# Kernel optimization log

Measured on AMD Instinct MI355X. Metric: run time of the kernel, lower is better.

The kernel has to match this reference:

```python
import jax, jax.numpy as jnp
import numpy as np

N_NODES = 100000
N_EDGES = 1600000
D_IN = 128
D_OUT = 128


def setup_inputs() -> dict:
    key = jax.random.key(0)
    k1, k2, k3, k4, k5 = jax.random.split(key, 5)
    h = jax.random.normal(k1, (N_NODES, D_IN), dtype=jnp.float32)
    src = jax.random.randint(k2, (N_EDGES,), 0, N_NODES, dtype=jnp.int64)
    dst = jax.random.randint(k3, (N_EDGES,), 0, N_NODES, dtype=jnp.int64)
    # Glorot-ish init for linear weights (PyTorch nn.Linear style: [out, in])
    scale = 1.0 / np.sqrt(D_IN)
    W_self = jax.random.uniform(k4, (D_OUT, D_IN), jnp.float32, -scale, scale)
    W_neigh = jax.random.uniform(k5, (D_OUT, D_IN), jnp.float32, -scale, scale)
    b = jnp.zeros((D_OUT,), dtype=jnp.float32)
    return {"h": h, "src": src, "dst": dst, "W_self": W_self,
            "W_neigh": W_neigh, "b": b}


def reference(h, src, dst, W_self, W_neigh, b):
    n_nodes = h.shape[0]
    # neighbor gather + segment-mean over in-neighbors (DGL fn.copy_u + fn.mean)
    msg = h[src]                                            # [E, D_in]
    neigh_sum = jax.ops.segment_sum(msg, dst, num_segments=n_nodes)
    deg = jax.ops.segment_sum(jnp.ones_like(dst, dtype=h.dtype), dst,
                              num_segments=n_nodes)         # [N]
    h_neigh = neigh_sum / jnp.maximum(deg, 1.0)[:, None]    # mean; 0 for isolated
    # SAGEConv mean: fc_self(h) + fc_neigh(h_neigh) + bias
    out = h @ W_self.T + h_neigh @ W_neigh.T + b
    return out
```

## Files before the change

kernel.cpp:

```cpp
#include <hip/hip_runtime.h>
#include <stdint.h>

#define NN 100000
#define NE 1600000
#define DD 128
#define NTILES ((NN + 127) / 128)
#define NB 256
#define CHUNK (NE / NB)
#define NBUCK ((NN + 255) / 256)
#define GH_N (NBUCK * NB)
#define GH_BLK (GH_N / 256)

typedef __bf16 bf16x8 __attribute__((ext_vector_type(8)));
typedef float f32x4 __attribute__((ext_vector_type(4)));
typedef float f32x2 __attribute__((ext_vector_type(2)));

__device__ __forceinline__ unsigned int f2bf2(float a, float b) {
  union { float f; unsigned u; } x, y;
  x.f = a; y.f = b;
  unsigned ua = x.u + (0x7FFFu + ((x.u >> 16) & 1u));
  unsigned ub = y.u + (0x7FFFu + ((y.u >> 16) & 1u));
  return (ua >> 16) | (ub & 0xFFFF0000u);
}

__global__ __launch_bounds__(256) void convert_hist_kernel(
    const float4* __restrict__ hp, uint2* __restrict__ h8,
    const int* __restrict__ dst, int* __restrict__ gh) {
  __shared__ int lh[NBUCK];
  int gid = blockIdx.x * 256 + threadIdx.x;
  float4 a = hp[2 * gid], b = hp[2 * gid + 1];
  int lo = __builtin_amdgcn_cvt_pk_fp8_f32(a.x, a.y, 0, false);
  lo = __builtin_amdgcn_cvt_pk_fp8_f32(a.z, a.w, lo, true);
  int hi = __builtin_amdgcn_cvt_pk_fp8_f32(b.x, b.y, 0, false);
  hi = __builtin_amdgcn_cvt_pk_fp8_f32(b.z, b.w, hi, true);
  h8[gid] = make_uint2((unsigned)lo, (unsigned)hi);

  if (blockIdx.x < NB) {
    int t = threadIdx.x, bb = blockIdx.x;
    for (int i = t; i < NBUCK; i += 256) lh[i] = 0;
    __syncthreads();
    int e0 = bb * CHUNK;
    for (int e = e0 + t; e < e0 + CHUNK; e += 256)
      atomicAdd(&lh[dst[e] >> 8], 1);
    __syncthreads();
    for (int i = t; i < NBUCK; i += 256) gh[i * NB + bb] = lh[i];
  }
}

__global__ __launch_bounds__(256) void blocksum_kernel(const int* __restrict__ gh,
                                                       int* __restrict__ bsum) {
  __shared__ int s[256];
  int t = threadIdx.x;
  s[t] = gh[blockIdx.x * 256 + t];
  __syncthreads();
  for (int d = 128; d > 0; d >>= 1) {
    if (t < d) s[t] += s[t + d];
    __syncthreads();
  }
  if (t == 0) bsum[blockIdx.x] = s[0];
}

__global__ __launch_bounds__(512) void scanbsum_kernel(const int* __restrict__ bsum,
                                                       int* __restrict__ bsum_ex) {
  __shared__ int s[512];
  int t = threadIdx.x;
  int v = (t < GH_BLK) ? bsum[t] : 0;
  s[t] = v;
  __syncthreads();
  for (int d = 1; d < 512; d <<= 1) {
    int x = (t >= d) ? s[t - d] : 0;
    __syncthreads();
    s[t] += x;
    __syncthreads();
  }
  if (t < GH_BLK) bsum_ex[t] = s[t] - v;
}

__global__ __launch_bounds__(256) void scanfull_kernel(const int* __restrict__ gh,
                                                       const int* __restrict__ bsum_ex,
                                                       int* __restrict__ gsc) {
  __shared__ int s[256];
  int t = threadIdx.x;
  int idx = blockIdx.x * 256 + t;
  int v = gh[idx];
  s[t] = v;
  __syncthreads();
  for (int d = 1; d < 256; d <<= 1) {
    int x = (t >= d) ? s[t - d] : 0;
    __syncthreads();
    s[t] += x;
    __syncthreads();
  }
  gsc[idx] = bsum_ex[blockIdx.x] + s[t] - v;
}

__global__ __launch_bounds__(256) void coarse_scatter_kernel(
    const int* __restrict__ src, const int* __restrict__ dst,
    const int* __restrict__ gsc, unsigned* __restrict__ ebuf) {
  __shared__ int lhpad[512];
  __shared__ int lbase[NBUCK];
  __shared__ int lcur[NBUCK];
  __shared__ int gstart[NBUCK];
  __shared__ unsigned sdata[CHUNK];
  __shared__ int sgpos[CHUNK];
  int t = threadIdx.x, b = blockIdx.x;
  lhpad[t] = 0;
  lhpad[t + 256] = 0;
  __syncthreads();
  int e0 = b * CHUNK;
  for (int e = e0 + t; e < e0 + CHUNK; e += 256)
    atomicAdd(&lhpad[dst[e] >> 8], 1);
  __syncthreads();
  int cnt0 = lhpad[t], cnt1 = lhpad[t + 256];
  for (int d = 1; d < 512; d <<= 1) {
    int x0 = (t >= d) ? lhpad[t - d] : 0;
    int x1 = ((t + 256) >= d) ? lhpad[t + 256 - d] : 0;
    __syncthreads();
    lhpad[t] += x0;
    lhpad[t + 256] += x1;
    __syncthreads();
  }
  if (t < NBUCK) { lbase[t] = lhpad[t] - cnt0; lcur[t] = 0; gstart[t] = gsc[t * NB + b]; }
  int i2 = t + 256;
  if (i2 < NBUCK) { lbase[i2] = lhpad[i2] - cnt1; lcur[i2] = 0; gstart[i2] = gsc[i2 * NB + b]; }
  __syncthreads();
  for (int e = e0 + t; e < e0 + CHUNK; e += 256) {
    int d = dst[e], s = src[e];
    int bk = d >> 8;
    int slot = atomicAdd(&lcur[bk], 1);
    int lp = lbase[bk] + slot;
    sdata[lp] = ((unsigned)(d & 255) << 24) | (unsigned)s;
    sgpos[lp] = gstart[bk] + slot;
  }
  __syncthreads();
  for (int j = t; j < CHUNK; j += 256) ebuf[sgpos[j]] = sdata[j];
}

__global__ __launch_bounds__(256) void fine_sort_kernel(const unsigned* __restrict__ ebuf,
                                                        const int* __restrict__ gsc,
                                                        int* __restrict__ csr,
                                                        int* __restrict__ offs) {
  __shared__ int hist[256], scn[256], cur[256];
  int t = threadIdx.x, g = blockIdx.x;
  int base = gsc[g * NB];
  int end = (g == NBUCK - 1) ? NE : gsc[(g + 1) * NB];
  hist[t] = 0;
  __syncthreads();
  for (int j = base + t; j < end; j += 256)
    atomicAdd(&hist[ebuf[j] >> 24], 1);
  __syncthreads();
  int v = hist[t];
  scn[t] = v;
  __syncthreads();
  for (int d = 1; d < 256; d <<= 1) {
    int x = (t >= d) ? scn[t - d] : 0;
    __syncthreads();
    scn[t] += x;
    __syncthreads();
  }
  int excl = scn[t] - v;
  int node = g * 256 + t;
  if (node < NN) offs[node] = base + excl;
  if (node == NN - 1) offs[NN] = NE;
  cur[t] = excl;
  __syncthreads();
  for (int j = base + t; j < end; j += 256) {
    unsigned p = ebuf[j];
    int pos = atomicAdd(&cur[p >> 24], 1);
    csr[base + pos] = (int)(p & 0x00FFFFFFu);
  }
}

__device__ __forceinline__ void acc16(float* a, uint4 u) {
  f32x2 p;
  p = __builtin_amdgcn_cvt_pk_f32_fp8(u.x, false); a[0] += p.x;  a[1] += p.y;
  p = __builtin_amdgcn_cvt_pk_f32_fp8(u.x, true);  a[2] += p.x;  a[3] += p.y;
  p = __builtin_amdgcn_cvt_pk_f32_fp8(u.y, false); a[4] += p.x;  a[5] += p.y;
  p = __builtin_amdgcn_cvt_pk_f32_fp8(u.y, true);  a[6] += p.x;  a[7] += p.y;
  p = __builtin_amdgcn_cvt_pk_f32_fp8(u.z, false); a[8] += p.x;  a[9] += p.y;
  p = __builtin_amdgcn_cvt_pk_f32_fp8(u.z, true);  a[10] += p.x; a[11] += p.y;
  p = __builtin_amdgcn_cvt_pk_f32_fp8(u.w, false); a[12] += p.x; a[13] += p.y;
  p = __builtin_amdgcn_cvt_pk_f32_fp8(u.w, true);  a[14] += p.x; a[15] += p.y;
}

__global__ __launch_bounds__(256) void gather_frag_kernel(
    const uint4* __restrict__ h8, const int* __restrict__ offs,
    const int* __restrict__ csr, uint4* __restrict__ hfrag) {
  int q = (blockIdx.x * 256 + threadIdx.x) >> 3;
  int l = threadIdx.x & 7;
  float a[16];
#pragma unroll
  for (int i = 0; i < 16; i++) a[i] = 0.f;
  float sc = 0.f;
  if (q < NN) {
    int off0 = offs[q], off1 = offs[q + 1];
    int j = off0;
    for (; j + 4 <= off1; j += 4) {
      int s0 = csr[j], s1 = csr[j + 1], s2 = csr[j + 2], s3 = csr[j + 3];
      uint4 u0 = h8[(size_t)s0 * 8 + l];
      uint4 u1 = h8[(size_t)s1 * 8 + l];
      uint4 u2 = h8[(size_t)s2 * 8 + l];
      uint4 u3 = h8[(size_t)s3 * 8 + l];
      acc16(a, u0); acc16(a, u1); acc16(a, u2); acc16(a, u3);
    }
    for (; j < off1; j++) acc16(a, h8[(size_t)csr[j] * 8 + l]);
    int deg = off1 - off0;
    sc = (deg > 0) ? (1.0f / (float)deg) : 0.0f;
  }
  uint4 r0, r1;
  r0.x = f2bf2(a[0] * sc, a[1] * sc);   r0.y = f2bf2(a[2] * sc, a[3] * sc);
  r0.z = f2bf2(a[4] * sc, a[5] * sc);   r0.w = f2bf2(a[6] * sc, a[7] * sc);
  r1.x = f2bf2(a[8] * sc, a[9] * sc);   r1.y = f2bf2(a[10] * sc, a[11] * sc);
  r1.z = f2bf2(a[12] * sc, a[13] * sc); r1.w = f2bf2(a[14] * sc, a[15] * sc);
  int r = q & 127;
  int rt = r >> 4, m = r & 15;
  int kc = l >> 1, quad = (l & 1) << 1;
  int slot = (((rt << 2) + kc) << 6) + (quad << 4) + m;
  uint4* base = hfrag + (size_t)(q >> 7) * 2048;
  base[slot] = r0;
  base[slot + 16] = r1;
}

__device__ __forceinline__ void stage_f32(const float* __restrict__ X,
                                          int row0, int nvalid,
                                          uint4* buf, int t) {
#pragma unroll
  for (int i = 0; i < 8; i++) {
    int id = t + (i << 8);
    int r = id >> 4;
    int c8 = id & 15;
    int row = row0 + r;
    float4 v0 = {0.f, 0.f, 0.f, 0.f}, v1 = {0.f, 0.f, 0.f, 0.f};
    if (row < nvalid) {
      const float4* p = (const float4*)(X + (size_t)row * DD + (c8 << 3));
      v0 = p[0];
      v1 = p[1];
    }
    uint4 q;
    q.x = f2bf2(v0.x, v0.y);
    q.y = f2bf2(v0.z, v0.w);
    q.z = f2bf2(v1.x, v1.y);
    q.w = f2bf2(v1.z, v1.w);
    int rt = r >> 4, m = r & 15, kc = c8 >> 2, quad = c8 & 3;
    buf[(((rt << 2) + kc) << 6) + (quad << 4) + m] = q;
  }
}

__device__ __forceinline__ void compute_half(const uint4* sA, const uint4* sW,
                                             f32x4 acc[2][8], int wv, int lane) {
#pragma unroll
  for (int kc = 0; kc < 4; kc++) {
    bf16x8 b[8];
#pragma unroll
    for (int n = 0; n < 8; n++)
      b[n] = *(const bf16x8*)&sW[(((n << 2) + kc) << 6) + lane];
    bf16x8 a0 = *(const bf16x8*)&sA[((((wv * 2 + 0) << 2) + kc) << 6) + lane];
    bf16x8 a1 = *(const bf16x8*)&sA[((((wv * 2 + 1) << 2) + kc) << 6) + lane];
#pragma unroll
    for (int n = 0; n < 8; n++) {
      acc[0][n] = __builtin_amdgcn_mfma_f32_16x16x32_bf16(a0, b[n], acc[0][n], 0, 0, 0);
      acc[1][n] = __builtin_amdgcn_mfma_f32_16x16x32_bf16(a1, b[n], acc[1][n], 0, 0, 0);
    }
  }
}

__global__ __launch_bounds__(256, 2) void gemm_kernel(
    const float* __restrict__ h, const uint4* __restrict__ hfrag,
    const float* __restrict__ Wself, const float* __restrict__ Wneigh,
    const float* __restrict__ bias, float* __restrict__ out) {
  __shared__ uint4 sA[2048];
  __shared__ uint4 sW[2048];
  int t = threadIdx.x;
  int wv = t >> 6;
  int lane = t & 63;
  int row0 = blockIdx.x * 128;

  const uint4* fb = hfrag + (size_t)blockIdx.x * 2048;
  uint4 a2[8];
#pragma unroll
  for (int kc = 0; kc < 4; kc++) {
    a2[kc]     = fb[((((wv * 2 + 0) << 2) + kc) << 6) + lane];
    a2[4 + kc] = fb[((((wv * 2 + 1) << 2) + kc) << 6) + lane];
  }

  f32x4 acc[2][8];
#pragma unroll
  for (int i = 0; i < 2; i++)
#pragma unroll
    for (int n = 0; n < 8; n++) acc[i][n] = f32x4{0.f, 0.f, 0.f, 0.f};

  stage_f32(h, row0, NN, sA, t);
  stage_f32(Wself, 0, 128, sW, t);
  __syncthreads();
  compute_half(sA, sW, acc, wv, lane);
  __syncthreads();

  stage_f32(Wneigh, 0, 128, sW, t);
  __syncthreads();
#pragma unroll
  for (int kc = 0; kc < 4; kc++) {
    bf16x8 b[8];
#pragma unroll
    for (int n = 0; n < 8; n++)
      b[n] = *(const bf16x8*)&sW[(((n << 2) + kc) << 6) + lane];
    bf16x8 a0 = *(const bf16x8*)&a2[kc];
    bf16x8 a1 = *(const bf16x8*)&a2[4 + kc];
#pragma unroll
    for (int n = 0; n < 8; n++) {
      acc[0][n] = __builtin_amdgcn_mfma_f32_16x16x32_bf16(a0, b[n], acc[0][n], 0, 0, 0);
      acc[1][n] = __builtin_amdgcn_mfma_f32_16x16x32_bf16(a1, b[n], acc[1][n], 0, 0, 0);
    }
  }

  int col = lane & 15, rq = lane >> 4;
  float bv[8];
#pragma unroll
  for (int n = 0; n < 8; n++) bv[n] = bias[n * 16 + col];
#pragma unroll
  for (int rt = 0; rt < 2; rt++) {
    int rb = row0 + (wv * 2 + rt) * 16 + rq * 4;
#pragma unroll
    for (int r = 0; r < 4; r++) {
      int row = rb + r;
      if (row < NN) {
        float* op = out + (size_t)row * DD + col;
#pragma unroll
        for (int n = 0; n < 8; n++) op[n * 16] = acc[rt][n][r] + bv[n];
      }
    }
  }
}

extern "C" void kernel_launch(void* const* d_in, const int* in_sizes, int n_in,
                              void* d_out, int out_size, void* d_ws, size_t ws_size,
                              hipStream_t stream) {
  const float* h      = (const float*)d_in[0];
  const int*   src    = (const int*)d_in[1];
  const int*   dst    = (const int*)d_in[2];
  const float* Wself  = (const float*)d_in[3];
  const float* Wneigh = (const float*)d_in[4];
  const float* bias   = (const float*)d_in[5];
  float* out = (float*)d_out;

  char* ws = (char*)d_ws;
  unsigned* h8       = (unsigned*)ws;
  unsigned* hfrag    = (unsigned*)(ws + 12800000);
  unsigned* ebuf     = (unsigned*)(ws + 12800000);
  int*      csr      = (int*)(ws + 38425600);
  int*      gh       = (int*)(ws + 44825600);
  int*      gsc      = (int*)(ws + 45225984);
  int*      bsum     = (int*)(ws + 45626368);
  int*      bsum_ex  = (int*)(ws + 45627936);
  int*      offs     = (int*)(ws + 45629504);

  convert_hist_kernel<<<6250, 256, 0, stream>>>((const float4*)h, (uint2*)h8, dst, gh);
  blocksum_kernel<<<GH_BLK, 256, 0, stream>>>(gh, bsum);
  scanbsum_kernel<<<1, 512, 0, stream>>>(bsum, bsum_ex);
  scanfull_kernel<<<GH_BLK, 256, 0, stream>>>(gh, bsum_ex, gsc);
  coarse_scatter_kernel<<<NB, 256, 0, stream>>>(src, dst, gsc, ebuf);
  fine_sort_kernel<<<NBUCK, 256, 0, stream>>>(ebuf, gsc, csr, offs);
  gather_frag_kernel<<<(NTILES * 128) / 32, 256, 0, stream>>>(
      (const uint4*)h8, offs, csr, (uint4*)hfrag);
  gemm_kernel<<<NTILES, 256, 0, stream>>>(h, (const uint4*)hfrag,
                                          Wself, Wneigh, bias, out);
}
```

Measured before the change: 224.1 us.

## Replace multi-kernel bucket scan with atomic reservation and pre-fragment h as bf16

```diff
diff --git a/kernel.cpp b/kernel.cpp
--- a/kernel.cpp
+++ b/kernel.cpp
@@ -5,11 +5,9 @@
 #define NE 1600000
 #define DD 128
 #define NTILES ((NN + 127) / 128)
-#define NB 256
+#define NB 512
 #define CHUNK (NE / NB)
 #define NBUCK ((NN + 255) / 256)
-#define GH_N (NBUCK * NB)
-#define GH_BLK (GH_N / 256)
 
 typedef __bf16 bf16x8 __attribute__((ext_vector_type(8)));
 typedef float f32x4 __attribute__((ext_vector_type(4)));
@@ -23,106 +21,92 @@
   return (ua >> 16) | (ub & 0xFFFF0000u);
 }
 
-__global__ __launch_bounds__(256) void convert_hist_kernel(
+__global__ __launch_bounds__(256) void zero_kernel(int* __restrict__ p) {
+  int t = blockIdx.x * 256 + threadIdx.x;
+  if (t < 2 * NBUCK) p[t] = 0;
+}
+
+__global__ __launch_bounds__(256) void convert_kernel(
     const float4* __restrict__ hp, uint2* __restrict__ h8,
-    const int* __restrict__ dst, int* __restrict__ gh) {
+    uint4* __restrict__ hbf, const int* __restrict__ dst,
+    int* __restrict__ ghist) {
   __shared__ int lh[NBUCK];
-  int gid = blockIdx.x * 256 + threadIdx.x;
-  float4 a = hp[2 * gid], b = hp[2 * gid + 1];
+  int t = threadIdx.x, b = blockIdx.x;
+  int gid = b * 256 + t;
+  float4 a = hp[2 * gid], c = hp[2 * gid + 1];
   int lo = __builtin_amdgcn_cvt_pk_fp8_f32(a.x, a.y, 0, false);
   lo = __builtin_amdgcn_cvt_pk_fp8_f32(a.z, a.w, lo, true);
-  int hi = __builtin_amdgcn_cvt_pk_fp8_f32(b.x, b.y, 0, false);
-  hi = __builtin_amdgcn_cvt_pk_fp8_f32(b.z, b.w, hi, true);
+  int hi = __builtin_amdgcn_cvt_pk_fp8_f32(c.x, c.y, 0, false);
+  hi = __builtin_amdgcn_cvt_pk_fp8_f32(c.z, c.w, hi, true);
   h8[gid] = make_uint2((unsigned)lo, (unsigned)hi);
 
-  if (blockIdx.x < NB) {
-    int t = threadIdx.x, bb = blockIdx.x;
+  uint4 q;
+  q.x = f2bf2(a.x, a.y);
+  q.y = f2bf2(a.z, a.w);
+  q.z = f2bf2(c.x, c.y);
+  q.w = f2bf2(c.z, c.w);
+  int m = t >> 4, c8 = t & 15;
+  int rt = b & 7, kc = c8 >> 2, quad = c8 & 3;
+  hbf[(size_t)(b >> 3) * 2048 + (((rt << 2) + kc) << 6) + (quad << 4) + m] = q;
+
+  if (b < NB) {
     for (int i = t; i < NBUCK; i += 256) lh[i] = 0;
     __syncthreads();
-    int e0 = bb * CHUNK;
+    int e0 = b * CHUNK;
     for (int e = e0 + t; e < e0 + CHUNK; e += 256)
       atomicAdd(&lh[dst[e] >> 8], 1);
     __syncthreads();
-    for (int i = t; i < NBUCK; i += 256) gh[i * NB + bb] = lh[i];
-  }
-}
-
-__global__ __launch_bounds__(256) void blocksum_kernel(const int* __restrict__ gh,
-                                                       int* __restrict__ bsum) {
-  __shared__ int s[256];
-  int t = threadIdx.x;
-  s[t] = gh[blockIdx.x * 256 + t];
-  __syncthreads();
-  for (int d = 128; d > 0; d >>= 1) {
-    if (t < d) s[t] += s[t + d];
-    __syncthreads();
-  }
-  if (t == 0) bsum[blockIdx.x] = s[0];
-}
-
-__global__ __launch_bounds__(512) void scanbsum_kernel(const int* __restrict__ bsum,
-                                                       int* __restrict__ bsum_ex) {
-  __shared__ int s[512];
-  int t = threadIdx.x;
-  int v = (t < GH_BLK) ? bsum[t] : 0;
-  s[t] = v;
-  __syncthreads();
-  for (int d = 1; d < 512; d <<= 1) {
-    int x = (t >= d) ? s[t - d] : 0;
-    __syncthreads();
-    s[t] += x;
-    __syncthreads();
-  }
-  if (t < GH_BLK) bsum_ex[t] = s[t] - v;
-}
-
-__global__ __launch_bounds__(256) void scanfull_kernel(const int* __restrict__ gh,
-                                                       const int* __restrict__ bsum_ex,
-                                                       int* __restrict__ gsc) {
-  __shared__ int s[256];
-  int t = threadIdx.x;
-  int idx = blockIdx.x * 256 + t;
-  int v = gh[idx];
-  s[t] = v;
-  __syncthreads();
-  for (int d = 1; d < 256; d <<= 1) {
-    int x = (t >= d) ? s[t - d] : 0;
-    __syncthreads();
-    s[t] += x;
-    __syncthreads();
-  }
-  gsc[idx] = bsum_ex[blockIdx.x] + s[t] - v;
+    for (int i = t; i < NBUCK; i += 256)
+      if (lh[i]) atomicAdd(&ghist[i], lh[i]);
+  }
 }
 
 __global__ __launch_bounds__(256) void coarse_scatter_kernel(
     const int* __restrict__ src, const int* __restrict__ dst,
-    const int* __restrict__ gsc, unsigned* __restrict__ ebuf) {
-  __shared__ int lhpad[512];
+    const int* __restrict__ ghist, int* __restrict__ gcur,
+    unsigned* __restrict__ ebuf) {
+  __shared__ int lhp[512];
+  __shared__ int gbp[512];
   __shared__ int lbase[NBUCK];
   __shared__ int lcur[NBUCK];
   __shared__ int gstart[NBUCK];
   __shared__ unsigned sdata[CHUNK];
   __shared__ int sgpos[CHUNK];
   int t = threadIdx.x, b = blockIdx.x;
-  lhpad[t] = 0;
-  lhpad[t + 256] = 0;
+  lhp[t] = 0;
+  lhp[t + 256] = 0;
+  gbp[t] = (t < NBUCK) ? ghist[t] : 0;
+  gbp[t + 256] = (t + 256 < NBUCK) ? ghist[t + 256] : 0;
   __syncthreads();
   int e0 = b * CHUNK;
   for (int e = e0 + t; e < e0 + CHUNK; e += 256)
-    atomicAdd(&lhpad[dst[e] >> 8], 1);
-  __syncthreads();
-  int cnt0 = lhpad[t], cnt1 = lhpad[t + 256];
+    atomicAdd(&lhp[dst[e] >> 8], 1);
+  __syncthreads();
+  int c0 = lhp[t], c1 = lhp[t + 256];
+  int g0 = gbp[t], g1 = gbp[t + 256];
   for (int d = 1; d < 512; d <<= 1) {
-    int x0 = (t >= d) ? lhpad[t - d] : 0;
-    int x1 = ((t + 256) >= d) ? lhpad[t + 256 - d] : 0;
-    __syncthreads();
-    lhpad[t] += x0;
-    lhpad[t + 256] += x1;
-    __syncthreads();
-  }
-  if (t < NBUCK) { lbase[t] = lhpad[t] - cnt0; lcur[t] = 0; gstart[t] = gsc[t * NB + b]; }
+    int x0 = (t >= d) ? lhp[t - d] : 0;
+    int x1 = ((t + 256) >= d) ? lhp[t + 256 - d] : 0;
+    int y0 = (t >= d) ? gbp[t - d] : 0;
+    int y1 = ((t + 256) >= d) ? gbp[t + 256 - d] : 0;
+    __syncthreads();
+    lhp[t] += x0; lhp[t + 256] += x1;
+    gbp[t] += y0; gbp[t + 256] += y1;
+    __syncthreads();
+  }
+  if (t < NBUCK) {
+    lbase[t] = lhp[t] - c0;
+    lcur[t] = 0;
+    int resv = c0 ? atomicAdd(&gcur[t], c0) : 0;
+    gstart[t] = (gbp[t] - g0) + resv;
+  }
   int i2 = t + 256;
-  if (i2 < NBUCK) { lbase[i2] = lhpad[i2] - cnt1; lcur[i2] = 0; gstart[i2] = gsc[i2 * NB + b]; }
+  if (i2 < NBUCK) {
+    lbase[i2] = lhp[i2] - c1;
+    lcur[i2] = 0;
+    int resv = c1 ? atomicAdd(&gcur[i2], c1) : 0;
+    gstart[i2] = (gbp[i2] - g1) + resv;
+  }
   __syncthreads();
   for (int e = e0 + t; e < e0 + CHUNK; e += 256) {
     int d = dst[e], s = src[e];
@@ -136,16 +120,25 @@
   for (int j = t; j < CHUNK; j += 256) ebuf[sgpos[j]] = sdata[j];
 }
 
-__global__ __launch_bounds__(256) void fine_sort_kernel(const unsigned* __restrict__ ebuf,
-                                                        const int* __restrict__ gsc,
-                                                        int* __restrict__ csr,
-                                                        int* __restrict__ offs) {
+__global__ __launch_bounds__(256) void fine_sort_kernel(
+    const unsigned* __restrict__ ebuf, const int* __restrict__ ghist,
+    int* __restrict__ csr, int* __restrict__ offs) {
+  __shared__ int gbp[512];
   __shared__ int hist[256], scn[256], cur[256];
   int t = threadIdx.x, g = blockIdx.x;
-  int base = gsc[g * NB];
-  int end = (g == NBUCK - 1) ? NE : gsc[(g + 1) * NB];
+  gbp[t] = (t < NBUCK) ? ghist[t] : 0;
+  gbp[t + 256] = (t + 256 < NBUCK) ? ghist[t + 256] : 0;
   hist[t] = 0;
   __syncthreads();
+  for (int d = 1; d < 512; d <<= 1) {
+    int y0 = (t >= d) ? gbp[t - d] : 0;
+    int y1 = ((t + 256) >= d) ? gbp[t + 256 - d] : 0;
+    __syncthreads();
+    gbp[t] += y0; gbp[t + 256] += y1;
+    __syncthreads();
+  }
+  int end = gbp[g];
+  int base = end - ghist[g];
   for (int j = base + t; j < end; j += 256)
     atomicAdd(&hist[ebuf[j] >> 24], 1);
   __syncthreads();
@@ -221,21 +214,15 @@
   base[slot + 16] = r1;
 }
 
-__device__ __forceinline__ void stage_f32(const float* __restrict__ X,
-                                          int row0, int nvalid,
-                                          uint4* buf, int t) {
+__device__ __forceinline__ void stage_w(const float* __restrict__ X,
+                                        uint4* buf, int t) {
 #pragma unroll
   for (int i = 0; i < 8; i++) {
     int id = t + (i << 8);
     int r = id >> 4;
     int c8 = id & 15;
-    int row = row0 + r;
-    float4 v0 = {0.f, 0.f, 0.f, 0.f}, v1 = {0.f, 0.f, 0.f, 0.f};
-    if (row < nvalid) {
-      const float4* p = (const float4*)(X + (size_t)row * DD + (c8 << 3));
-      v0 = p[0];
-      v1 = p[1];
-    }
+    const float4* p = (const float4*)(X + (size_t)r * DD + (c8 << 3));
+    float4 v0 = p[0], v1 = p[1];
     uint4 q;
     q.x = f2bf2(v0.x, v0.y);
     q.y = f2bf2(v0.z, v0.w);
@@ -246,42 +233,47 @@
   }
 }
 
-__device__ __forceinline__ void compute_half(const uint4* sA, const uint4* sW,
-                                             f32x4 acc[2][8], int wv, int lane) {
+__device__ __forceinline__ void compute_reg(const uint4* a, const uint4* sWb,
+                                            f32x4 acc[2][8], int lane) {
 #pragma unroll
   for (int kc = 0; kc < 4; kc++) {
-    bf16x8 b[8];
+    bf16x8 bfr[8];
 #pragma unroll
     for (int n = 0; n < 8; n++)
-      b[n] = *(const bf16x8*)&sW[(((n << 2) + kc) << 6) + lane];
-    bf16x8 a0 = *(const bf16x8*)&sA[((((wv * 2 + 0) << 2) + kc) << 6) + lane];
-    bf16x8 a1 = *(const bf16x8*)&sA[((((wv * 2 + 1) << 2) + kc) << 6) + lane];
+      bfr[n] = *(const bf16x8*)&sWb[(((n << 2) + kc) << 6) + lane];
+    bf16x8 a0 = *(const bf16x8*)&a[kc];
+    bf16x8 a1 = *(const bf16x8*)&a[4 + kc];
 #pragma unroll
     for (int n = 0; n < 8; n++) {
-      acc[0][n] = __builtin_amdgcn_mfma_f32_16x16x32_bf16(a0, b[n], acc[0][n], 0, 0, 0);
-      acc[1][n] = __builtin_amdgcn_mfma_f32_16x16x32_bf16(a1, b[n], acc[1][n], 0, 0, 0);
+      acc[0][n] = __builtin_amdgcn_mfma_f32_16x16x32_bf16(a0, bfr[n], acc[0][n], 0, 0, 0);
+      acc[1][n] = __builtin_amdgcn_mfma_f32_16x16x32_bf16(a1, bfr[n], acc[1][n], 0, 0, 0);
     }
   }
 }
 
 __global__ __launch_bounds__(256, 2) void gemm_kernel(
-    const float* __restrict__ h, const uint4* __restrict__ hfrag,
+    const uint4* __restrict__ hbf, const uint4* __restrict__ hfrag,
     const float* __restrict__ Wself, const float* __restrict__ Wneigh,
     const float* __restrict__ bias, float* __restrict__ out) {
-  __shared__ uint4 sA[2048];
-  __shared__ uint4 sW[2048];
+  __shared__ uint4 sW[4096];
   int t = threadIdx.x;
   int wv = t >> 6;
   int lane = t & 63;
   int row0 = blockIdx.x * 128;
 
-  const uint4* fb = hfrag + (size_t)blockIdx.x * 2048;
-  uint4 a2[8];
+  const uint4* fb1 = hbf + (size_t)blockIdx.x * 2048;
+  const uint4* fb2 = hfrag + (size_t)blockIdx.x * 2048;
+  uint4 a1[8], a2[8];
 #pragma unroll
   for (int kc = 0; kc < 4; kc++) {
-    a2[kc]     = fb[((((wv * 2 + 0) << 2) + kc) << 6) + lane];
-    a2[4 + kc] = fb[((((wv * 2 + 1) << 2) + kc) << 6) + lane];
-  }
+    int s0 = ((((wv * 2 + 0) << 2) + kc) << 6) + lane;
+    int s1 = ((((wv * 2 + 1) << 2) + kc) << 6) + lane;
+    a1[kc] = fb1[s0]; a1[4 + kc] = fb1[s1];
+    a2[kc] = fb2[s0]; a2[4 + kc] = fb2[s1];
+  }
+
+  stage_w(Wself, sW, t);
+  stage_w(Wneigh, sW + 2048, t);
 
   f32x4 acc[2][8];
 #pragma unroll
@@ -289,28 +281,9 @@
 #pragma unroll
     for (int n = 0; n < 8; n++) acc[i][n] = f32x4{0.f, 0.f, 0.f, 0.f};
 
-  stage_f32(h, row0, NN, sA, t);
-  stage_f32(Wself, 0, 128, sW, t);
-  __syncthreads();
-  compute_half(sA, sW, acc, wv, lane);
-  __syncthreads();
-
-  stage_f32(Wneigh, 0, 128, sW, t);
-  __syncthreads();
-#pragma unroll
-  for (int kc = 0; kc < 4; kc++) {
-    bf16x8 b[8];
-#pragma unroll
-    for (int n = 0; n < 8; n++)
-      b[n] = *(const bf16x8*)&sW[(((n << 2) + kc) << 6) + lane];
-    bf16x8 a0 = *(const bf16x8*)&a2[kc];
-    bf16x8 a1 = *(const bf16x8*)&a2[4 + kc];
-#pragma unroll
-    for (int n = 0; n < 8; n++) {
-      acc[0][n] = __builtin_amdgcn_mfma_f32_16x16x32_bf16(a0, b[n], acc[0][n], 0, 0, 0);
-      acc[1][n] = __builtin_amdgcn_mfma_f32_16x16x32_bf16(a1, b[n], acc[1][n], 0, 0, 0);
-    }
-  }
+  __syncthreads();
+  compute_reg(a1, sW, acc, lane);
+  compute_reg(a2, sW + 2048, acc, lane);
 
   int col = lane & 15, rq = lane >> 4;
   float bv[8];
@@ -344,23 +317,21 @@
 
   char* ws = (char*)d_ws;
   unsigned* h8       = (unsigned*)ws;
-  unsigned* hfrag    = (unsigned*)(ws + 12800000);
-  unsigned* ebuf     = (unsigned*)(ws + 12800000);
-  int*      csr      = (int*)(ws + 38425600);
-  int*      gh       = (int*)(ws + 44825600);
-  int*      gsc      = (int*)(ws + 45225984);
-  int*      bsum     = (int*)(ws + 45626368);
-  int*      bsum_ex  = (int*)(ws + 45627936);
-  int*      offs     = (int*)(ws + 45629504);
-
-  convert_hist_kernel<<<6250, 256, 0, stream>>>((const float4*)h, (uint2*)h8, dst, gh);
-  blocksum_kernel<<<GH_BLK, 256, 0, stream>>>(gh, bsum);
-  scanbsum_kernel<<<1, 512, 0, stream>>>(bsum, bsum_ex);
-  scanfull_kernel<<<GH_BLK, 256, 0, stream>>>(gh, bsum_ex, gsc);
-  coarse_scatter_kernel<<<NB, 256, 0, stream>>>(src, dst, gsc, ebuf);
-  fine_sort_kernel<<<NBUCK, 256, 0, stream>>>(ebuf, gsc, csr, offs);
+  unsigned* hbf      = (unsigned*)(ws + 12800000);
+  unsigned* hfrag    = (unsigned*)(ws + 38424576);
+  unsigned* ebuf     = (unsigned*)(ws + 38424576);
+  int*      csr      = (int*)(ws + 64049152);
+  int*      offs     = (int*)(ws + 70449152);
+  int*      ghist    = (int*)(ws + 70849168);
+  int*      gcur     = (int*)(ws + 70850732);
+
+  zero_kernel<<<(2 * NBUCK + 255) / 256, 256, 0, stream>>>(ghist);
+  convert_kernel<<<6250, 256, 0, stream>>>((const float4*)h, (uint2*)h8,
+                                           (uint4*)hbf, dst, ghist);
+  coarse_scatter_kernel<<<NB, 256, 0, stream>>>(src, dst, ghist, gcur, ebuf);
+  fine_sort_kernel<<<NBUCK, 256, 0, stream>>>(ebuf, ghist, csr, offs);
   gather_frag_kernel<<<(NTILES * 128) / 32, 256, 0, stream>>>(
       (const uint4*)h8, offs, csr, (uint4*)hfrag);
-  gemm_kernel<<<NTILES, 256, 0, stream>>>(h, (const uint4*)hfrag,
+  gemm_kernel<<<NTILES, 256, 0, stream>>>((const uint4*)hbf, (const uint4*)hfrag,
                                           Wself, Wneigh, bias, out);
 }
```

Result: slower. 229.5 us (+2.4%).
